# Kernel optimization log

Measured on AMD Instinct MI355X. Metric: run time of the kernel, lower is better.

The kernel has to match this reference:

```python
import jax, jax.numpy as jnp
import numpy as np

B, N, E = 4, 10000, 160000
IN, OUT, H, ED = 64, 128, 2, 1
SLOPE = 0.2  # GATv2Conv default negative_slope


def _seg_softmax(logits, seg, n):
    # logits: [Ef, H]; softmax over edges sharing the same dst node, per head
    m = jax.ops.segment_max(logits, seg, num_segments=n)
    e = jnp.exp(logits - m[seg])
    d = jax.ops.segment_sum(e, seg, num_segments=n)
    return e / d[seg]


def setup_inputs() -> dict:
    key = jax.random.key(0)
    ks = jax.random.split(key, 10)
    s = 0.05
    return {
        "node_feats": jax.random.normal(ks[0], (B, N, IN), jnp.float32),
        "edge_index": jax.random.randint(ks[1], (2, E), 0, N, dtype=jnp.int64),
        "edge_attr": jax.random.normal(ks[2], (E, ED), jnp.float32),
        "Wl": jax.random.normal(ks[3], (IN, H * OUT), jnp.float32) * s,
        "bl": jax.random.normal(ks[4], (H * OUT,), jnp.float32) * s,
        "Wr": jax.random.normal(ks[5], (IN, H * OUT), jnp.float32) * s,
        "br": jax.random.normal(ks[6], (H * OUT,), jnp.float32) * s,
        "We": jax.random.normal(ks[7], (ED, H * OUT), jnp.float32) * s,
        "att": jax.random.normal(ks[8], (H, OUT), jnp.float32) * s,
        "bias": jax.random.normal(ks[9], (H * OUT,), jnp.float32) * s,
    }


def reference(node_feats, edge_index, edge_attr, Wl, bl, Wr, br, We, att, bias):
    src, dst = edge_index[0], edge_index[1]
    # PyG add_self_loops(fill_value='mean'): self-loop attr = mean of incoming edge attrs per node
    ones = jnp.ones((E,), edge_attr.dtype)
    deg = jax.ops.segment_sum(ones, dst, num_segments=N)
    loop_attr = jax.ops.segment_sum(edge_attr, dst, num_segments=N) / jnp.maximum(deg, 1.0)[:, None]
    sl = jnp.arange(N)
    src_f = jnp.concatenate([src, sl])           # [Ef] with Ef = E + N
    dst_f = jnp.concatenate([dst, sl])
    e_feat = (jnp.concatenate([edge_attr, loop_attr], axis=0) @ We).reshape(-1, H, OUT)  # [Ef,H,C]

    xl = (node_feats @ Wl + bl).reshape(B, N, H, OUT)  # lin_l(x)
    xr = (node_feats @ Wr + br).reshape(B, N, H, OUT)  # lin_r(x)

    # GATv2: score on leaky_relu(x_l[src] + x_r[dst] + lin_edge(e))
    msg = jax.nn.leaky_relu(xl[:, src_f] + xr[:, dst_f] + e_feat[None], SLOPE)  # [B,Ef,H,C]
    logits = jnp.einsum('behc,hc->beh', msg, att)                               # [B,Ef,H]
    alpha = jax.vmap(lambda l: _seg_softmax(l, dst_f, N))(logits)               # [B,Ef,H]

    weighted = alpha[..., None] * xl[:, src_f]                                  # [B,Ef,H,C]
    out = jax.vmap(lambda w: jax.ops.segment_sum(w, dst_f, num_segments=N))(weighted)  # [B,N,H,C]
    return out.reshape(B, N, H * OUT) + bias
```

## Files before the change

### kernel.cpp

```cpp
#include <hip/hip_runtime.h>
#include <hip/hip_bf16.h>

#define BQ 4
#define NN 10000
#define EE 160000
#define HC 256
#define SLOPEK 0.2f
#define CAPE 128

typedef __attribute__((ext_vector_type(8))) short bf16x8;
typedef __attribute__((ext_vector_type(4))) float f32x4;
typedef __attribute__((ext_vector_type(2))) float f32x2;

__device__ __forceinline__ unsigned short f2bf(float f) {
    unsigned int u = __float_as_uint(f);
    u = (u + 0x7FFFu + ((u >> 16) & 1u)) >> 16;
    return (unsigned short)u;
}
__device__ __forceinline__ f32x2 bf2(unsigned int u) {
    return (f32x2){__uint_as_float(u << 16), __uint_as_float(u & 0xFFFF0000u)};
}

__global__ __launch_bounds__(256) void k_wpack(
    const float* __restrict__ Wl, const float* __restrict__ bl,
    const float* __restrict__ Wr, const float* __restrict__ br,
    unsigned short* __restrict__ wp, float* __restrict__ bp,
    int* __restrict__ zbase)
{
    if (blockIdx.x >= 130) {
        const int i = (blockIdx.x - 130) * 256 + threadIdx.x;
        if (i < 2 * NN) zbase[i] = 0;
        return;
    }
    const int tid = blockIdx.x * 256 + threadIdx.x;
    if (tid < 32768) {
        const int j  = tid & 7;
        const int l  = (tid >> 3) & 63;
        const int s  = (tid >> 9) & 1;
        const int ct = tid >> 10;
        const int col = ct * 16 + (l & 15);
        const int kk  = s * 32 + ((l >> 4) << 3) + j;
        const float w = (col < 256) ? Wl[kk * 256 + col] : Wr[kk * 256 + (col - 256)];
        wp[tid] = f2bf(w);
    } else if (tid < 32768 + 512) {
        const int c = tid - 32768;
        bp[c] = (c < 256) ? bl[c] : br[c - 256];
    }
}

__global__ __launch_bounds__(256) void k_pre(
    const float* __restrict__ x, const unsigned short* __restrict__ wp,
    const float* __restrict__ bp,
    unsigned short* __restrict__ xl, unsigned short* __restrict__ xr,
    const int* __restrict__ ei, const float* __restrict__ ea,
    int* __restrict__ cnt, float* __restrict__ asum,
    int* __restrict__ cmeta)
{
    __shared__ unsigned short st[64][264];

    if (blockIdx.x >= 625) {
        const int e = (blockIdx.x - 625) * 256 + threadIdx.x;
        const int   sn = ei[e];
        const int   d  = ei[EE + e];
        const float a  = ea[e];
        const int pos  = atomicAdd(&cnt[d], 1);
        atomicAdd(&asum[d], a);
        if (pos < CAPE - 1)
            cmeta[d * CAPE + pos] = (sn << 16) | (int)f2bf(a);
        return;
    }
    const int t = threadIdx.x;
    const int w = t >> 6, l = t & 63;
    const int row0 = blockIdx.x * 64 + w * 16;
    const int arow = row0 + (l & 15);
    const float* xp = x + (size_t)arow * 64 + ((l >> 4) << 3);

    bf16x8 a[2];
#pragma unroll
    for (int s = 0; s < 2; ++s) {
        const float4 lo = *reinterpret_cast<const float4*>(xp + s * 32);
        const float4 hi = *reinterpret_cast<const float4*>(xp + s * 32 + 4);
        union { bf16x8 v; unsigned short u[8]; } tt;
        tt.u[0] = f2bf(lo.x); tt.u[1] = f2bf(lo.y); tt.u[2] = f2bf(lo.z); tt.u[3] = f2bf(lo.w);
        tt.u[4] = f2bf(hi.x); tt.u[5] = f2bf(hi.y); tt.u[6] = f2bf(hi.z); tt.u[7] = f2bf(hi.w);
        a[s] = tt.v;
    }
    const int colb = l & 15;
    const int rsub = (l >> 4) << 2;

    for (int h = 0; h < 2; ++h) {
        for (int g4 = 0; g4 < 4; ++g4) {
            f32x4 acc[4] = {{0.f,0.f,0.f,0.f},{0.f,0.f,0.f,0.f},
                            {0.f,0.f,0.f,0.f},{0.f,0.f,0.f,0.f}};
#pragma unroll
            for (int c = 0; c < 4; ++c) {
                const int ct = h * 16 + g4 * 4 + c;
                const bf16x8 b0 = *reinterpret_cast<const bf16x8*>(wp + (((ct * 2 + 0) * 64 + l) << 3));
                const bf16x8 b1 = *reinterpret_cast<const bf16x8*>(wp + (((ct * 2 + 1) * 64 + l) << 3));
                acc[c] = __builtin_amdgcn_mfma_f32_16x16x32_bf16(a[0], b0, acc[c], 0, 0, 0);
                acc[c] = __builtin_amdgcn_mfma_f32_16x16x32_bf16(a[1], b1, acc[c], 0, 0, 0);
            }
#pragma unroll
            for (int c = 0; c < 4; ++c) {
                const int colh = (g4 * 4 + c) * 16 + colb;
                const float bv = bp[h * 256 + colh];
#pragma unroll
                for (int r = 0; r < 4; ++r)
                    st[w * 16 + rsub + r][colh] = f2bf(acc[c][r] + bv);
            }
        }
        __syncthreads();
        unsigned short* __restrict__ dstb = h ? xr : xl;
        for (int rr = (t >> 5); rr < 64; rr += 8) {
            const size_t row = blockIdx.x * 64 + rr;
            const uint4 v = *reinterpret_cast<const uint4*>(&st[rr][(t & 31) * 8]);
            *reinterpret_cast<uint4*>(dstb + (row << 8) + (t & 31) * 8) = v;
        }
        __syncthreads();
    }
}

__global__ __launch_bounds__(256) void k_gat(
    const unsigned short* __restrict__ xl, const unsigned short* __restrict__ xr,
    const int* __restrict__ cnt, const float* __restrict__ asum,
    const int* __restrict__ cmeta,
    const float* __restrict__ We, const float* __restrict__ att,
    const float* __restrict__ bias, float* __restrict__ outp)
{
    const int t  = threadIdx.x;
    const int wv = t >> 6, ln = t & 63;
    const int batch = blockIdx.x & 3;
    const int n  = (blockIdx.x >> 2) * 4 + wv;
    const int ch0 = ln * 4;

    int dg0 = cnt[n];
    if (dg0 > 63) dg0 = 63;
    const int dg = __builtin_amdgcn_readfirstlane(dg0);
    int mp = cmeta[n * CAPE + ln];
    if (ln == dg)
        mp = (n << 16) | (int)f2bf(asum[n] / fmaxf((float)dg, 1.0f));
    const int ntot = dg + 1;

    f32x2 we2[2], at2[2], xr2[2], acc2[2];
    {
        const float4 w4 = *reinterpret_cast<const float4*>(We + ch0);
        const float4 a4 = *reinterpret_cast<const float4*>(att + ch0);
        we2[0] = (f32x2){w4.x, w4.y}; we2[1] = (f32x2){w4.z, w4.w};
        at2[0] = (f32x2){a4.x, a4.y}; at2[1] = (f32x2){a4.z, a4.w};
        const uint2 r0 = *reinterpret_cast<const uint2*>(
            xr + (((size_t)(batch * NN + n)) << 8) + ch0);
        xr2[0] = bf2(r0.x); xr2[1] = bf2(r0.y);
    }
    const f32x2 km1 = {SLOPEK - 1.f, SLOPEK - 1.f};
    const f32x2 z2  = {0.f, 0.f};
    acc2[0] = z2; acc2[1] = z2;
    float sh = 0.f;

    const unsigned short* __restrict__ xlb = xl + (((size_t)batch * NN) << 8) + ch0;

    uint2 A0, A1, A2, A3;
    float ea0, ea1, ea2, ea3;

#define LOADSLOT(S, IDX) do { \
        const int ii_ = (IDX); \
        const int ic_ = ii_ < dg ? ii_ : dg; \
        const int sc_ = __builtin_amdgcn_readlane(mp, ic_); \
        ea##S = __uint_as_float(((unsigned int)sc_) << 16); \
        A##S = *reinterpret_cast<const uint2*>(xlb + ((size_t)(sc_ >> 16) << 8)); \
    } while (0)

    auto edgeC = [&](const uint2& A, float a0) {
        f32x2 xv2[2];
        xv2[0] = bf2(A.x); xv2[1] = bf2(A.y);

        const f32x2 a02 = {a0, a0};
        f32x2 q2 = z2;
#pragma unroll
        for (int j = 0; j < 2; ++j) {
            f32x2 s = xv2[j] + xr2[j];
            f32x2 v = __builtin_elementwise_fma(a02, we2[j], s);
            f32x2 vm = __builtin_elementwise_min(v, z2);
            v = __builtin_elementwise_fma(km1, vm, v);
            q2 = __builtin_elementwise_fma(v, at2[j], q2);
        }
        float p = q2.x + q2.y;
        p += __shfl_xor(p, 1);
        p += __shfl_xor(p, 2);
        p += __shfl_xor(p, 4);
        p += __shfl_xor(p, 8);
        p += __shfl_xor(p, 16);
        const float e = __expf(p);
        sh += e;
        const f32x2 e2 = {e, e};
        acc2[0] = __builtin_elementwise_fma(e2, xv2[0], acc2[0]);
        acc2[1] = __builtin_elementwise_fma(e2, xv2[1], acc2[1]);
    };

    LOADSLOT(0, 0);
    LOADSLOT(1, 1);
    LOADSLOT(2, 2);

    int i = 0;
    for (; i + 3 < ntot; i += 4) {
        LOADSLOT(3, i + 3); edgeC(A0, ea0);
        LOADSLOT(0, i + 4); edgeC(A1, ea1);
        LOADSLOT(1, i + 5); edgeC(A2, ea2);
        LOADSLOT(2, i + 6); edgeC(A3, ea3);
    }
    if (i     < ntot) edgeC(A0, ea0);
    if (i + 1 < ntot) edgeC(A1, ea1);
    if (i + 2 < ntot) edgeC(A2, ea2);
#undef LOADSLOT

    const float inv = 1.0f / sh;
    const float4 b4 = *reinterpret_cast<const float4*>(bias + ch0);
    float4 o;
    o.x = fmaf(acc2[0].x, inv, b4.x);
    o.y = fmaf(acc2[0].y, inv, b4.y);
    o.z = fmaf(acc2[1].x, inv, b4.z);
    o.w = fmaf(acc2[1].y, inv, b4.w);
    *reinterpret_cast<float4*>(outp + (((size_t)(batch * NN + n)) << 8) + ch0) = o;
}

extern "C" void kernel_launch(void* const* d_in, const int* in_sizes, int n_in,
                              void* d_out, int out_size, void* d_ws, size_t ws_size,
                              hipStream_t stream)
{
    (void)in_sizes; (void)n_in; (void)out_size; (void)ws_size;
    const float* x    = (const float*)d_in[0];
    const int*   ei   = (const int*)d_in[1];
    const float* ea   = (const float*)d_in[2];
    const float* Wl   = (const float*)d_in[3];
    const float* bl   = (const float*)d_in[4];
    const float* Wr   = (const float*)d_in[5];
    const float* br   = (const float*)d_in[6];
    const float* We   = (const float*)d_in[7];
    const float* att  = (const float*)d_in[8];
    const float* bias = (const float*)d_in[9];
    float* outp = (float*)d_out;

    const size_t R = (size_t)BQ * NN;
    unsigned short* xl16 = (unsigned short*)d_ws;
    unsigned short* xr16 = xl16 + R * HC;
    int*   cnt   = (int*)(xr16 + R * HC);
    float* asum  = (float*)(cnt + NN);
    int*   cmeta = (int*)(asum + NN);
    unsigned short* wp = (unsigned short*)(cmeta + (size_t)NN * CAPE);
    float* bp    = (float*)(wp + 32768);

    k_wpack<<<130 + (2 * NN + 255) / 256, 256, 0, stream>>>(Wl, bl, Wr, br, wp, bp, cnt);
    k_pre  <<<1250, 256, 0, stream>>>(x, wp, bp, xl16, xr16,
                                      ei, ea, cnt, asum, cmeta);
    k_gat  <<<NN, 256, 0, stream>>>(xl16, xr16, cnt, asum, cmeta,
                                    We, att, bias, outp);
}
```

Before: 97.09 us.

## Process two edges per wavefront using half-waves with 16-byte gathers

Splits each 64-lane wavefront into two 32-lane halves that work on different incoming edges at once. Each lane now covers 8 channels with a 16-byte bf16 gather instead of 4 channels with 8 bytes, and the per-head attention reduction needs one fewer shuffle stage. At the end the halves' softmax sums and accumulators are merged with a cross-half shuffle, and each half writes half of the outputs. The cmeta stride is cut from 128 to 64. This costs more registers per lane, a padded odd tail that is masked with a zero weight, and two readlanes per load slot.

```diff
diff --git a/kernel.cpp b/kernel.cpp
--- a/kernel.cpp
+++ b/kernel.cpp
@@ -6,7 +6,7 @@
 #define EE 160000
 #define HC 256
 #define SLOPEK 0.2f
-#define CAPE 128
+#define CAPE 64
 
 typedef __attribute__((ext_vector_type(8))) short bf16x8;
 typedef __attribute__((ext_vector_type(4))) float f32x4;
@@ -131,95 +131,119 @@
     const int wv = t >> 6, ln = t & 63;
     const int batch = blockIdx.x & 3;
     const int n  = (blockIdx.x >> 2) * 4 + wv;
-    const int ch0 = ln * 4;
+    const int hi = ln >> 5;
+    const int ch0 = (ln & 31) * 8;
 
     int dg0 = cnt[n];
-    if (dg0 > 63) dg0 = 63;
+    if (dg0 > CAPE - 1) dg0 = CAPE - 1;
     const int dg = __builtin_amdgcn_readfirstlane(dg0);
     int mp = cmeta[n * CAPE + ln];
     if (ln == dg)
         mp = (n << 16) | (int)f2bf(asum[n] / fmaxf((float)dg, 1.0f));
     const int ntot = dg + 1;
 
-    f32x2 we2[2], at2[2], xr2[2], acc2[2];
+    f32x2 we2[4], at2[4], xr2[4], acc2[4];
     {
-        const float4 w4 = *reinterpret_cast<const float4*>(We + ch0);
-        const float4 a4 = *reinterpret_cast<const float4*>(att + ch0);
-        we2[0] = (f32x2){w4.x, w4.y}; we2[1] = (f32x2){w4.z, w4.w};
-        at2[0] = (f32x2){a4.x, a4.y}; at2[1] = (f32x2){a4.z, a4.w};
-        const uint2 r0 = *reinterpret_cast<const uint2*>(
+        const float4* Wp = reinterpret_cast<const float4*>(We + ch0);
+        const float4* Ap = reinterpret_cast<const float4*>(att + ch0);
+#pragma unroll
+        for (int j = 0; j < 2; ++j) {
+            const float4 w4 = Wp[j], a4 = Ap[j];
+            we2[2*j+0] = (f32x2){w4.x, w4.y};
+            we2[2*j+1] = (f32x2){w4.z, w4.w};
+            at2[2*j+0] = (f32x2){a4.x, a4.y};
+            at2[2*j+1] = (f32x2){a4.z, a4.w};
+        }
+        const uint4 r0 = *reinterpret_cast<const uint4*>(
             xr + (((size_t)(batch * NN + n)) << 8) + ch0);
-        xr2[0] = bf2(r0.x); xr2[1] = bf2(r0.y);
+        xr2[0] = bf2(r0.x); xr2[1] = bf2(r0.y); xr2[2] = bf2(r0.z); xr2[3] = bf2(r0.w);
     }
     const f32x2 km1 = {SLOPEK - 1.f, SLOPEK - 1.f};
     const f32x2 z2  = {0.f, 0.f};
-    acc2[0] = z2; acc2[1] = z2;
+#pragma unroll
+    for (int k = 0; k < 4; ++k) acc2[k] = z2;
     float sh = 0.f;
 
-    const unsigned short* __restrict__ xlb = xl + (((size_t)batch * NN) << 8) + ch0;
-
-    uint2 A0, A1, A2, A3;
+    const unsigned short* __restrict__ xlb =
+        xl + (((size_t)batch * NN) << 8) + ch0;
+
+    uint4 A0, A1, A2, A3;
     float ea0, ea1, ea2, ea3;
 
-#define LOADSLOT(S, IDX) do { \
-        const int ii_ = (IDX); \
-        const int ic_ = ii_ < dg ? ii_ : dg; \
-        const int sc_ = __builtin_amdgcn_readlane(mp, ic_); \
-        ea##S = __uint_as_float(((unsigned int)sc_) << 16); \
-        A##S = *reinterpret_cast<const uint2*>(xlb + ((size_t)(sc_ >> 16) << 8)); \
+#define LOADSLOT(S, I) do { \
+        const int iA_ = (I) < dg ? (I) : dg; \
+        const int iB_ = (I) + 1 < dg ? (I) + 1 : dg; \
+        const int mA_ = __builtin_amdgcn_readlane(mp, iA_); \
+        const int mB_ = __builtin_amdgcn_readlane(mp, iB_); \
+        const int mm_ = hi ? mB_ : mA_; \
+        ea##S = __uint_as_float(((unsigned int)mm_) << 16); \
+        A##S = *reinterpret_cast<const uint4*>(xlb + ((size_t)(mm_ >> 16) << 8)); \
     } while (0)
 
-    auto edgeC = [&](const uint2& A, float a0) {
-        f32x2 xv2[2];
-        xv2[0] = bf2(A.x); xv2[1] = bf2(A.y);
+    auto edgeC = [&](const uint4& A, float a0, int idx) {
+        f32x2 xv2[4];
+        xv2[0] = bf2(A.x); xv2[1] = bf2(A.y); xv2[2] = bf2(A.z); xv2[3] = bf2(A.w);
 
         const f32x2 a02 = {a0, a0};
-        f32x2 q2 = z2;
-#pragma unroll
-        for (int j = 0; j < 2; ++j) {
+        f32x2 qa = z2, qb = z2;
+#pragma unroll
+        for (int j = 0; j < 4; ++j) {
             f32x2 s = xv2[j] + xr2[j];
             f32x2 v = __builtin_elementwise_fma(a02, we2[j], s);
             f32x2 vm = __builtin_elementwise_min(v, z2);
             v = __builtin_elementwise_fma(km1, vm, v);
-            q2 = __builtin_elementwise_fma(v, at2[j], q2);
-        }
+            if (j & 1) qb = __builtin_elementwise_fma(v, at2[j], qb);
+            else       qa = __builtin_elementwise_fma(v, at2[j], qa);
+        }
+        const f32x2 q2 = qa + qb;
         float p = q2.x + q2.y;
         p += __shfl_xor(p, 1);
         p += __shfl_xor(p, 2);
         p += __shfl_xor(p, 4);
         p += __shfl_xor(p, 8);
-        p += __shfl_xor(p, 16);
-        const float e = __expf(p);
+        float e = __expf(p);
+        if (idx + hi >= ntot) e = 0.f;
         sh += e;
         const f32x2 e2 = {e, e};
-        acc2[0] = __builtin_elementwise_fma(e2, xv2[0], acc2[0]);
-        acc2[1] = __builtin_elementwise_fma(e2, xv2[1], acc2[1]);
+#pragma unroll
+        for (int j = 0; j < 4; ++j)
+            acc2[j] = __builtin_elementwise_fma(e2, xv2[j], acc2[j]);
     };
 
     LOADSLOT(0, 0);
-    LOADSLOT(1, 1);
-    LOADSLOT(2, 2);
+    LOADSLOT(1, 2);
+    LOADSLOT(2, 4);
 
     int i = 0;
-    for (; i + 3 < ntot; i += 4) {
-        LOADSLOT(3, i + 3); edgeC(A0, ea0);
-        LOADSLOT(0, i + 4); edgeC(A1, ea1);
-        LOADSLOT(1, i + 5); edgeC(A2, ea2);
-        LOADSLOT(2, i + 6); edgeC(A3, ea3);
-    }
-    if (i     < ntot) edgeC(A0, ea0);
-    if (i + 1 < ntot) edgeC(A1, ea1);
-    if (i + 2 < ntot) edgeC(A2, ea2);
+    for (; i + 6 < ntot; i += 8) {
+        LOADSLOT(3, i + 6);  edgeC(A0, ea0, i);
+        LOADSLOT(0, i + 8);  edgeC(A1, ea1, i + 2);
+        LOADSLOT(1, i + 10); edgeC(A2, ea2, i + 4);
+        LOADSLOT(2, i + 12); edgeC(A3, ea3, i + 6);
+    }
+    if (i     < ntot) edgeC(A0, ea0, i);
+    if (i + 2 < ntot) edgeC(A1, ea1, i + 2);
+    if (i + 4 < ntot) edgeC(A2, ea2, i + 4);
 #undef LOADSLOT
 
+    sh += __shfl_xor(sh, 32);
+#pragma unroll
+    for (int j = 0; j < 4; ++j) {
+        acc2[j].x += __shfl_xor(acc2[j].x, 32);
+        acc2[j].y += __shfl_xor(acc2[j].y, 32);
+    }
+
     const float inv = 1.0f / sh;
-    const float4 b4 = *reinterpret_cast<const float4*>(bias + ch0);
+    const f32x2 s0 = hi ? acc2[2] : acc2[0];
+    const f32x2 s1 = hi ? acc2[3] : acc2[1];
+    const float4 b4 = *reinterpret_cast<const float4*>(bias + ch0 + hi * 4);
     float4 o;
-    o.x = fmaf(acc2[0].x, inv, b4.x);
-    o.y = fmaf(acc2[0].y, inv, b4.y);
-    o.z = fmaf(acc2[1].x, inv, b4.z);
-    o.w = fmaf(acc2[1].y, inv, b4.w);
-    *reinterpret_cast<float4*>(outp + (((size_t)(batch * NN + n)) << 8) + ch0) = o;
+    o.x = fmaf(s0.x, inv, b4.x);
+    o.y = fmaf(s0.y, inv, b4.y);
+    o.z = fmaf(s1.x, inv, b4.z);
+    o.w = fmaf(s1.y, inv, b4.w);
+    *reinterpret_cast<float4*>(
+        outp + (((size_t)(batch * NN + n)) << 8) + ch0 + hi * 4) = o;
 }
 
 extern "C" void kernel_launch(void* const* d_in, const int* in_sizes, int n_in,
```

New measurement: 89.09 us. 8.2% less time.
